# Performance work log

Hardware: AMD Instinct MI355X
Metric: run time of the kernel (lower is better)

Reference implementation:

```python
import jax, jax.numpy as jnp
import numpy as np

G, N, F_IN, D, R, E, L = 512, 128, 64, 128, 4, 1572864, 2  # graphs, nodes/graph, in-feat, embed, relations, edges, gnn layers


def setup_inputs() -> dict:
    key = jax.random.key(0)
    ks = jax.random.split(key, 8)
    x = jax.random.normal(ks[0], (G * N, F_IN), jnp.float32)
    # edges are within-graph (disjoint batched graph, as built by batch_to_gd)
    gid = jax.random.randint(ks[1], (E,), 0, G)
    loc = jax.random.randint(ks[2], (2, E), 0, N)
    edge_index = gid[None, :] * N + loc  # [2, E] (src, dst)
    edge_attr = jax.random.randint(ks[3], (E,), 0, R)
    W_emb = jax.random.normal(ks[4], (F_IN, D), jnp.float32) / np.sqrt(F_IN)
    b_emb = jnp.zeros((D,), jnp.float32)
    W_root = jax.random.normal(ks[5], (L, D, D), jnp.float32) / np.sqrt(D)
    W_rel = jax.random.normal(ks[6], (L, R, D, D), jnp.float32) / np.sqrt(D)
    bias = jnp.zeros((L, D), jnp.float32)
    return {"x": x, "edge_index": edge_index, "edge_attr": edge_attr,
            "W_emb": W_emb, "b_emb": b_emb, "W_root": W_root, "W_rel": W_rel, "bias": bias}


def rgcn_layer(h, edge_index, edge_attr, W_root_l, W_rel_l, bias_l):
    # PyG RGCNConv: out_i = h_i @ W_root + sum_r mean_{j in N_r(i)} (h_j @ W_r) + bias
    n = h.shape[0]
    xr = jnp.einsum('nd,rde->rne', h, W_rel_l)          # [R, n, D] per-relation transform
    src, dst = edge_index[0], edge_index[1]
    msg = xr[edge_attr, src]                             # [E, D] gather per edge
    seg = dst * R + edge_attr                            # combined (node, relation) segment id
    summed = jax.ops.segment_sum(msg, seg, num_segments=n * R)
    cnt = jax.ops.segment_sum(jnp.ones((msg.shape[0],), h.dtype), seg, num_segments=n * R)
    mean = summed / jnp.maximum(cnt, 1.0)[:, None]       # per-relation mean aggregation
    agg = mean.reshape(n, R, -1).sum(axis=1)             # sum over relations
    return h @ W_root_l + agg + bias_l


def reference(x, edge_index, edge_attr, W_emb, b_emb, W_root, W_rel, bias):
    h = x @ W_emb + b_emb                                # embedding_linear
    for l in range(L):                                   # mp_rounds = 1 per layer
        h = jax.nn.relu(rgcn_layer(h, edge_index, edge_attr, W_root[l], W_rel[l], bias[l]))
    # split into per-graph chunks of N nodes and max-pool over nodes
    return jnp.max(h.reshape(G, N, -1), axis=1)          # [G, D]
```

## Files before the change

### kernel.cpp

```cpp
#include <hip/hip_runtime.h>

constexpr int GG    = 512;
constexpr int NPG   = 128;
constexpr int FIN   = 64;
constexpr int DD    = 128;
constexpr int RR    = 4;
constexpr int NN    = GG * NPG;
constexpr int EE    = 1572864;
constexpr int SLC   = 4096;
constexpr int HSTR  = 136;
constexpr int BPAD  = 32;

typedef __attribute__((ext_vector_type(8))) _Float16 f16x8;
typedef __attribute__((ext_vector_type(2))) _Float16 f16x2;
typedef __attribute__((ext_vector_type(4))) float f32x4;
typedef unsigned short u16;
typedef unsigned int   u32;

__device__ __forceinline__ u16 f16b(float x) {
    _Float16 h = (_Float16)x;
    return __builtin_bit_cast(u16, h);
}
__device__ __forceinline__ f16x2 as2(u32 w) { return __builtin_bit_cast(f16x2, w); }

__device__ __forceinline__ void gl_lds16(const void* g, void* l) {
    __builtin_amdgcn_global_load_lds((const __attribute__((address_space(1))) u32*)g,
                                     (__attribute__((address_space(3))) u32*)l, 16, 0, 0);
}


__global__ __launch_bounds__(256, 2) void k_front(const int* __restrict__ ei,
                                                  const int* __restrict__ ea,
                                                  u32* __restrict__ bcur,
                                                  u16* __restrict__ binned,
                                                  const float* __restrict__ W_root,
                                                  const float* __restrict__ W_rel,
                                                  const float* __restrict__ W_emb,
                                                  u16* __restrict__ wtH) {
    __shared__ u32 sRec[4096];
    __shared__ int bh[512];
    __shared__ int lcur[512];
    __shared__ int lstart[512];
    __shared__ int gbase[512];
    __shared__ int wt4[4];
    __shared__ float tile[32 * 129];
    int tid = threadIdx.x;
    int bid = blockIdx.x;

    if (bid < 384) {
        int e0 = bid * 4096;
        bh[tid] = 0; bh[tid + 256] = 0;
        __syncthreads();
        for (int i = 0; i < 16; ++i) {
            int e = e0 + i * 256 + tid;
            int src = ei[e];
            int dst = ei[EE + e];
            int a   = ea[e];
            int g   = dst >> 7;
            u32 rec = (u32)(src & 127) | ((u32)(dst & 127) << 7) | ((u32)a << 14);
            sRec[i * 256 + tid] = rec | ((u32)g << 16);
            atomicAdd(&bh[g], 1);
        }
        __syncthreads();
        int c0 = bh[2 * tid], c1 = bh[2 * tid + 1];
        int s  = c0 + c1;
        int v  = s;
        int lane = tid & 63, wv = tid >> 6;
#pragma unroll
        for (int o = 1; o < 64; o <<= 1) {
            int t = __shfl_up(v, o);
            if (lane >= o) v += t;
        }
        if (lane == 63) wt4[wv] = v;
        gbase[2 * tid]     = (2 * tid) * SLC +
                             (int)atomicAdd(&bcur[(2 * tid) * BPAD], (u32)c0);
        gbase[2 * tid + 1] = (2 * tid + 1) * SLC +
                             (int)atomicAdd(&bcur[(2 * tid + 1) * BPAD], (u32)c1);
        __syncthreads();
        int base = 0;
#pragma unroll
        for (int w = 0; w < 4; ++w)
            if (w < wv) base += wt4[w];
        int ex = base + v - s;
        lstart[2 * tid]     = ex;
        lstart[2 * tid + 1] = ex + c0;
        lcur[2 * tid]       = ex;
        lcur[2 * tid + 1]   = ex + c0;
        __syncthreads();
        u32* sorted = (u32*)tile;
        for (int i = 0; i < 16; ++i) {
            u32 r = sRec[i * 256 + tid];
            int pos = atomicAdd(&lcur[r >> 16], 1);
            sorted[pos] = r;
        }
        __syncthreads();
        for (int i = 0; i < 16; ++i) {
            int p = i * 256 + tid;
            u32 r = sorted[p];
            int g = r >> 16;
            binned[gbase[g] + (p - lstart[g])] = (u16)(r & 0xFFFFu);
        }
    } else if (bid < 424) {
        int pb = bid - 384;
        int mat = pb >> 2;
        int k0 = (pb & 3) * 32;
        int l = mat / 5, m5 = mat - l * 5;
        const float* Wsrc = (m5 == 0) ? (W_root + l * 16384)
                                      : (W_rel + (size_t)(l * RR + (m5 - 1)) * 16384);
        for (int i = 0; i < 16; ++i) {
            int k = k0 + (tid >> 7) + i * 2;
            int n = tid & 127;
            tile[(k - k0) * 129 + n] = Wsrc[k * 128 + n];
        }
        __syncthreads();
        for (int i = 0; i < 16; ++i) {
            int kk = tid & 31;
            int n  = (tid >> 5) + i * 8;
            wtH[mat * 16384 + n * 128 + k0 + kk] = f16b(tile[kk * 129 + n]);
        }
    } else {
        int k0 = (bid - 424) * 32;
        for (int i = 0; i < 16; ++i) {
            int k = k0 + (tid >> 7) + i * 2;
            int n = tid & 127;
            tile[(k - k0) * 129 + n] = W_emb[k * 128 + n];
        }
        __syncthreads();
        for (int i = 0; i < 16; ++i) {
            int kk = tid & 31;
            int n  = (tid >> 5) + i * 8;
            wtH[163840 + n * 64 + k0 + kk] = f16b(tile[kk * 129 + n]);
        }
    }
}


__global__ __launch_bounds__(512, 4) void k_fused(const float* __restrict__ x,
                                                  const float* __restrict__ b_emb,
                                                  float* __restrict__ outF,
                                                  const u16* __restrict__ wtH,
                                                  const float* __restrict__ bias,
                                                  const u16* __restrict__ binned,
                                                  const u32* __restrict__ bcur) {
    __shared__ __align__(16) u16 hG[128 * HSTR];
    __shared__ __align__(16) u16 sQ[2][8192];
    __shared__ __align__(16) u16 sIdx[SLC];
    __shared__ int   sOffs[512];
    __shared__ int   sCnt[512];
    __shared__ float sInv[512];

    int tid  = threadIdx.x;
    int wave = tid >> 6, lane = tid & 63;
    int mm   = lane & 15;
    int qd   = lane >> 4;
    int gr   = blockIdx.x;
    int row0g = gr * NPG;
    int strip = wave * 16;
    const u16* wtE = wtH + 163840;

    auto stage = [&](int step, int bufi) {
        const u16* src = wtH + (step >> 1) * 16384 + (step & 1) * 64;
#pragma unroll
        for (int i = 0; i < 2; ++i) {
            int u = i * 512 + tid;
            int n = u >> 3, j = u & 7;
            gl_lds16(src + n * 128 + ((j ^ (n & 7)) * 8), &sQ[bufi][u * 8]);
        }
    };
    auto stageE = [&](int bufi) {
#pragma unroll
        for (int i = 0; i < 2; ++i) {
            int u = i * 512 + tid;
            int n = u >> 3, j = u & 7;
            gl_lds16(wtE + n * 64 + ((j ^ (n & 7)) * 8), &sQ[bufi][u * 8]);
        }
    };

    f32x4 acc[8];
    auto mfma_half = [&](int bufi, f16x8 A0, f16x8 A1) {
        const u16* buf = sQ[bufi];
#pragma unroll
        for (int nt = 0; nt < 8; ++nt) {
            int n = nt * 16 + mm;
            int g0 = n * 8 + ((0 * 4 + qd) ^ (n & 7));
            int g1 = n * 8 + ((1 * 4 + qd) ^ (n & 7));
            f16x8 B0 = *(const f16x8*)&buf[g0 * 8];
            f16x8 B1 = *(const f16x8*)&buf[g1 * 8];
            f32x4 a = acc[nt];
            a = __builtin_amdgcn_mfma_f32_16x16x32_f16(A0, B0, a, 0, 0, 0);
            a = __builtin_amdgcn_mfma_f32_16x16x32_f16(A1, B1, a, 0, 0, 0);
            acc[nt] = a;
        }
    };

    auto gather = [&](int rel, f16x8* AH) {
        int key = (rel << 7) + strip + mm;
        int r0 = sOffs[key];
        int r1 = sCnt[key];
        _Float16 hs = (_Float16)sInv[key];
        f16x2 sv; sv[0] = hs; sv[1] = hs;
        int cb = qd * 8;
        f16x2 ax[16];
#pragma unroll
        for (int i = 0; i < 16; ++i) ax[i] = (f16x2){(_Float16)0.f, (_Float16)0.f};
        auto add8 = [&](int ks, uint4 u) {
            ax[ks * 4 + 0] += as2(u.x);
            ax[ks * 4 + 1] += as2(u.y);
            ax[ks * 4 + 2] += as2(u.z);
            ax[ks * 4 + 3] += as2(u.w);
        };
        int j = r0;
        for (; j + 2 <= r1; j += 2) {
            int rb0 = (int)sIdx[j]     * HSTR + cb;
            int rb1 = (int)sIdx[j + 1] * HSTR + cb;
            uint4 a0 = *(const uint4*)&hG[rb0];
            uint4 a1 = *(const uint4*)&hG[rb0 + 32];
            uint4 a2 = *(const uint4*)&hG[rb0 + 64];
            uint4 a3 = *(const uint4*)&hG[rb0 + 96];
            uint4 b0 = *(const uint4*)&hG[rb1];
            uint4 b1 = *(const uint4*)&hG[rb1 + 32];
            uint4 b2 = *(const uint4*)&hG[rb1 + 64];
            uint4 b3 = *(const uint4*)&hG[rb1 + 96];
            add8(0, a0); add8(1, a1); add8(2, a2); add8(3, a3);
            add8(0, b0); add8(1, b1); add8(2, b2); add8(3, b3);
        }
        if (j < r1) {
            int rb = (int)sIdx[j] * HSTR + cb;
            uint4 a0 = *(const uint4*)&hG[rb];
            uint4 a1 = *(const uint4*)&hG[rb + 32];
            uint4 a2 = *(const uint4*)&hG[rb + 64];
            uint4 a3 = *(const uint4*)&hG[rb + 96];
            add8(0, a0); add8(1, a1); add8(2, a2); add8(3, a3);
        }
#pragma unroll
        for (int q = 0; q < 4; ++q) {
            union { u32 w[4]; f16x8 v; } o;
#pragma unroll
            for (int t = 0; t < 4; ++t) {
                f16x2 r = ax[q * 4 + t] * sv;
                o.w[t] = __builtin_bit_cast(u32, r);
            }
            AH[q] = o.v;
        }
    };

    stageE(0);
    int cnt = (int)bcur[gr * BPAD];
    if (cnt > SLC) cnt = SLC;
    uint4 myRec = *(const uint4*)&binned[gr * SLC + tid * 8];
    sCnt[tid] = 0;
    __syncthreads();
    int base8 = tid * 8;
#pragma unroll
    for (int i = 0; i < 8; ++i) {
        if (base8 + i < cnt) {
            u32 w = ((const u32*)&myRec)[i >> 1];
            u32 rec = (i & 1) ? (w >> 16) : (w & 0xFFFFu);
            atomicAdd(&sCnt[rec >> 7], 1);
        }
    }
    __syncthreads();
    int c = sCnt[tid];
    int v = c;
#pragma unroll
    for (int o = 1; o < 64; o <<= 1) {
        int t = __shfl_up(v, o);
        if (lane >= o) v += t;
    }
    int* wtot = (int*)sIdx;
    if (lane == 63) wtot[wave] = v;
    __syncthreads();
    int base = 0;
#pragma unroll
    for (int w = 0; w < 8; ++w) {
        int tw = wtot[w];
        if (w < wave) base += tw;
    }
    int ex = base + v - c;
    sOffs[tid] = ex;
    sCnt[tid]  = ex;
    sInv[tid]  = 1.0f / (float)(c > 0 ? c : 1);
    __syncthreads();
#pragma unroll
    for (int i = 0; i < 8; ++i) {
        if (base8 + i < cnt) {
            u32 w = ((const u32*)&myRec)[i >> 1];
            u32 rec = (i & 1) ? (w >> 16) : (w & 0xFFFFu);
            int pos = atomicAdd(&sCnt[rec >> 7], 1);
            sIdx[pos] = (u16)(rec & 127u);
        }
    }
    __syncthreads();

    {
#pragma unroll
        for (int nt = 0; nt < 8; ++nt) {
            float bv = b_emb[nt * 16 + mm];
            acc[nt] = (f32x4){bv, bv, bv, bv};
        }
        f16x8 AE[2];
#pragma unroll
        for (int ks = 0; ks < 2; ++ks) {
            const float* xp = &x[(size_t)(row0g + strip + mm) * FIN + ks * 32 + qd * 8];
            float4 a = *(const float4*)xp;
            float4 b = *(const float4*)(xp + 4);
            union { u32 w[4]; f16x8 v; } o;
            o.w[0] = (u32)f16b(a.x) | ((u32)f16b(a.y) << 16);
            o.w[1] = (u32)f16b(a.z) | ((u32)f16b(a.w) << 16);
            o.w[2] = (u32)f16b(b.x) | ((u32)f16b(b.y) << 16);
            o.w[3] = (u32)f16b(b.z) | ((u32)f16b(b.w) << 16);
            AE[ks] = o.v;
        }
        stage(0, 1);
        mfma_half(0, AE[0], AE[1]);
#pragma unroll
        for (int nt = 0; nt < 8; ++nt)
#pragma unroll
            for (int r = 0; r < 4; ++r)
                hG[(strip + qd * 4 + r) * HSTR + nt * 16 + mm] =
                    f16b(acc[nt][r]);
        __syncthreads();
    }

    for (int L = 0; L < 2; ++L) {
        const float* bl = bias + L * DD;
#pragma unroll
        for (int i = 0; i < 8; ++i) acc[i] = (f32x4){0.f, 0.f, 0.f, 0.f};

        f16x8 AH[4];
#pragma unroll
        for (int ks = 0; ks < 4; ++ks)
            AH[ks] = *(const f16x8*)&hG[(strip + mm) * HSTR + ks * 32 + qd * 8];

        for (int m = 0; m < 5; ++m) {
#pragma unroll
            for (int h = 0; h < 2; ++h) {
                int s = L * 10 + m * 2 + h;
                if (s + 1 < 20) stage(s + 1, s & 1);
                mfma_half((s + 1) & 1, AH[h * 2], AH[h * 2 + 1]);
                __syncthreads();
            }
            if (m < 4) gather(m, AH);
        }

        if (L == 0) {
#pragma unroll
            for (int nt = 0; nt < 8; ++nt) {
                float bv = bl[nt * 16 + mm];
#pragma unroll
                for (int r = 0; r < 4; ++r)
                    hG[(strip + qd * 4 + r) * HSTR + nt * 16 + mm] =
                        f16b(fmaxf(acc[nt][r] + bv, 0.f));
            }
            __syncthreads();
        } else {
            float* red = (float*)sIdx;
#pragma unroll
            for (int nt = 0; nt < 8; ++nt) {
                float bv = bl[nt * 16 + mm];
                float vv = fmaxf(fmaxf(acc[nt][0], acc[nt][1]),
                                 fmaxf(acc[nt][2], acc[nt][3])) + bv;
                vv = fmaxf(vv, 0.f);
                vv = fmaxf(vv, __shfl_xor(vv, 16));
                vv = fmaxf(vv, __shfl_xor(vv, 32));
                if (lane < 16) red[wave * 128 + nt * 16 + mm] = vv;
            }
            __syncthreads();
            if (tid < 128) {
                float mx = red[tid];
#pragma unroll
                for (int w = 1; w < 8; ++w) mx = fmaxf(mx, red[w * 128 + tid]);
                outF[gr * DD + tid] = mx;
            }
        }
    }
}


extern "C" void kernel_launch(void* const* d_in, const int* in_sizes, int n_in,
                              void* d_out, int out_size, void* d_ws, size_t ws_size,
                              hipStream_t stream) {
    const float* x      = (const float*)d_in[0];
    const int*   ei     = (const int*)  d_in[1];
    const int*   ea     = (const int*)  d_in[2];
    const float* W_emb  = (const float*)d_in[3];
    const float* b_emb  = (const float*)d_in[4];
    const float* W_root = (const float*)d_in[5];
    const float* W_rel  = (const float*)d_in[6];
    const float* bias   = (const float*)d_in[7];
    float* out = (float*)d_out;

    char* p = (char*)d_ws;
    u32* bcur   = (u32*)p; p += (size_t)512 * BPAD * 4;
    u16* binned = (u16*)p; p += (size_t)GG * SLC * 2;
    u16* wtH    = (u16*)p; p += (size_t)(10 * 16384 + 8192) * 2;

    (void)hipMemsetAsync(bcur, 0, (size_t)512 * BPAD * 4, stream);

    k_front<<<426, 256, 0, stream>>>(ei, ea, bcur, binned,
                                     W_root, W_rel, W_emb, wtH);
    k_fused<<<GG, 512, 0, stream>>>(x, b_emb, out, wtH, bias, binned, bcur);
}
```

Baseline: 162.2 us.

## Read weight B-operands directly from global memory instead of LDS double-buffer staging

Removes the LDS double-buffered weight staging (global_load_lds plus per-half barriers) and has each wave load MFMA B fragments straight from global/L2. This frees 32 KB of LDS and drops the per-step __syncthreads, and occupancy is raised from 4 to 6 blocks per CU via launch bounds. In exchange every wave re-fetches the full weight matrices from cache with uncoalesced-ish 16-byte loads, which adds L2/L1 traffic and latency. A leftover no-op lambda is also included.

```diff
diff --git a/kernel.cpp b/kernel.cpp
--- a/kernel.cpp
+++ b/kernel.cpp
@@ -22,11 +22,6 @@
     return __builtin_bit_cast(u16, h);
 }
 __device__ __forceinline__ f16x2 as2(u32 w) { return __builtin_bit_cast(f16x2, w); }
-
-__device__ __forceinline__ void gl_lds16(const void* g, void* l) {
-    __builtin_amdgcn_global_load_lds((const __attribute__((address_space(1))) u32*)g,
-                                     (__attribute__((address_space(3))) u32*)l, 16, 0, 0);
-}
 
 
 __global__ __launch_bounds__(256, 2) void k_front(const int* __restrict__ ei,
@@ -135,7 +130,7 @@
 }
 
 
-__global__ __launch_bounds__(512, 4) void k_fused(const float* __restrict__ x,
+__global__ __launch_bounds__(512, 6) void k_fused(const float* __restrict__ x,
                                                   const float* __restrict__ b_emb,
                                                   float* __restrict__ outF,
                                                   const u16* __restrict__ wtH,
@@ -143,7 +138,6 @@
                                                   const u16* __restrict__ binned,
                                                   const u32* __restrict__ bcur) {
     __shared__ __align__(16) u16 hG[128 * HSTR];
-    __shared__ __align__(16) u16 sQ[2][8192];
     __shared__ __align__(16) u16 sIdx[SLC];
     __shared__ int   sOffs[512];
     __shared__ int   sCnt[512];
@@ -158,40 +152,17 @@
     int strip = wave * 16;
     const u16* wtE = wtH + 163840;
 
-    auto stage = [&](int step, int bufi) {
-        const u16* src = wtH + (step >> 1) * 16384 + (step & 1) * 64;
-#pragma unroll
-        for (int i = 0; i < 2; ++i) {
-            int u = i * 512 + tid;
-            int n = u >> 3, j = u & 7;
-            gl_lds16(src + n * 128 + ((j ^ (n & 7)) * 8), &sQ[bufi][u * 8]);
+    f32x4 acc[8];
+
+    auto mat_mm = [&](const u16* base) {
+        const u16* bl = base + mm * 128 + qd * 8;
+#pragma unroll
+        for (int ks = 0; ks < 4; ++ks) {
+            f16x8 A;
+            (void)A;
         }
     };
-    auto stageE = [&](int bufi) {
-#pragma unroll
-        for (int i = 0; i < 2; ++i) {
-            int u = i * 512 + tid;
-            int n = u >> 3, j = u & 7;
-            gl_lds16(wtE + n * 64 + ((j ^ (n & 7)) * 8), &sQ[bufi][u * 8]);
-        }
-    };
-
-    f32x4 acc[8];
-    auto mfma_half = [&](int bufi, f16x8 A0, f16x8 A1) {
-        const u16* buf = sQ[bufi];
-#pragma unroll
-        for (int nt = 0; nt < 8; ++nt) {
-            int n = nt * 16 + mm;
-            int g0 = n * 8 + ((0 * 4 + qd) ^ (n & 7));
-            int g1 = n * 8 + ((1 * 4 + qd) ^ (n & 7));
-            f16x8 B0 = *(const f16x8*)&buf[g0 * 8];
-            f16x8 B1 = *(const f16x8*)&buf[g1 * 8];
-            f32x4 a = acc[nt];
-            a = __builtin_amdgcn_mfma_f32_16x16x32_f16(A0, B0, a, 0, 0, 0);
-            a = __builtin_amdgcn_mfma_f32_16x16x32_f16(A1, B1, a, 0, 0, 0);
-            acc[nt] = a;
-        }
-    };
+    (void)mat_mm;
 
     auto gather = [&](int rel, f16x8* AH) {
         int key = (rel << 7) + strip + mm;
@@ -244,7 +215,6 @@
         }
     };
 
-    stageE(0);
     int cnt = (int)bcur[gr * BPAD];
     if (cnt > SLC) cnt = SLC;
     uint4 myRec = *(const uint4*)&binned[gr * SLC + tid * 8];
@@ -311,8 +281,14 @@
             o.w[3] = (u32)f16b(b.z) | ((u32)f16b(b.w) << 16);
             AE[ks] = o.v;
         }
-        stage(0, 1);
-        mfma_half(0, AE[0], AE[1]);
+        const u16* bl = wtE + mm * 64 + qd * 8;
+#pragma unroll
+        for (int ks = 0; ks < 2; ++ks)
+#pragma unroll
+            for (int nt = 0; nt < 8; ++nt) {
+                f16x8 B = *(const f16x8*)&bl[nt * 16 * 64 + ks * 32];
+                acc[nt] = __builtin_amdgcn_mfma_f32_16x16x32_f16(AE[ks], B, acc[nt], 0, 0, 0);
+            }
 #pragma unroll
         for (int nt = 0; nt < 8; ++nt)
 #pragma unroll
@@ -333,15 +309,17 @@
             AH[ks] = *(const f16x8*)&hG[(strip + mm) * HSTR + ks * 32 + qd * 8];
 
         for (int m = 0; m < 5; ++m) {
-#pragma unroll
-            for (int h = 0; h < 2; ++h) {
-                int s = L * 10 + m * 2 + h;
-                if (s + 1 < 20) stage(s + 1, s & 1);
-                mfma_half((s + 1) & 1, AH[h * 2], AH[h * 2 + 1]);
-                __syncthreads();
-            }
+            const u16* mb = wtH + (size_t)(L * 5 + m) * 16384 + mm * 128 + qd * 8;
+#pragma unroll
+            for (int ks = 0; ks < 4; ++ks)
+#pragma unroll
+                for (int nt = 0; nt < 8; ++nt) {
+                    f16x8 B = *(const f16x8*)&mb[nt * 16 * 128 + ks * 32];
+                    acc[nt] = __builtin_amdgcn_mfma_f32_16x16x32_f16(AH[ks], B, acc[nt], 0, 0, 0);
+                }
             if (m < 4) gather(m, AH);
         }
+        __syncthreads();
 
         if (L == 0) {
 #pragma unroll
```

Result: slower. 282.1 us (+74.0%).

## Process two graphs per 1024-thread block sharing staged weight tiles

Applied to the files above, without the earlier changes.

Each block now handles two graphs with 1024 threads, with each half keeping its own node features, edge index bins and counters in LDS. The double-buffered weight tiles are shared by both halves and staged with one load per thread, which halves weight traffic and staging work per graph. The cost is block-wide barriers across both graphs, a grid of only 256 blocks on a GPU with many CUs, and more LDS per block, which may lower occupancy and leave load imbalance between the two graphs.

```diff
diff --git a/kernel.cpp b/kernel.cpp
--- a/kernel.cpp
+++ b/kernel.cpp
@@ -135,45 +135,45 @@
 }
 
 
-__global__ __launch_bounds__(512, 4) void k_fused(const float* __restrict__ x,
-                                                  const float* __restrict__ b_emb,
-                                                  float* __restrict__ outF,
-                                                  const u16* __restrict__ wtH,
-                                                  const float* __restrict__ bias,
-                                                  const u16* __restrict__ binned,
-                                                  const u32* __restrict__ bcur) {
-    __shared__ __align__(16) u16 hG[128 * HSTR];
+__global__ __launch_bounds__(1024, 4) void k_fused(const float* __restrict__ x,
+                                                   const float* __restrict__ b_emb,
+                                                   float* __restrict__ outF,
+                                                   const u16* __restrict__ wtH,
+                                                   const float* __restrict__ bias,
+                                                   const u16* __restrict__ binned,
+                                                   const u32* __restrict__ bcur) {
+    __shared__ __align__(16) u16 hG[2][128 * HSTR];
     __shared__ __align__(16) u16 sQ[2][8192];
-    __shared__ __align__(16) u16 sIdx[SLC];
-    __shared__ int   sOffs[512];
-    __shared__ int   sCnt[512];
-    __shared__ float sInv[512];
+    __shared__ __align__(16) u16 sIdx[2][SLC];
+    __shared__ int   sOffs[2][512];
+    __shared__ int   sCnt[2][512];
+    __shared__ float sInv[2][512];
 
     int tid  = threadIdx.x;
-    int wave = tid >> 6, lane = tid & 63;
+    int half = tid >> 9;
+    int htid = tid & 511;
+    int wave = htid >> 6, lane = tid & 63;
     int mm   = lane & 15;
     int qd   = lane >> 4;
-    int gr   = blockIdx.x;
+    int gr   = (blockIdx.x << 1) | half;
     int row0g = gr * NPG;
     int strip = wave * 16;
     const u16* wtE = wtH + 163840;
 
+    u16*   hGh   = hG[half];
+    u16*   sIdxh = sIdx[half];
+    int*   sOffsh = sOffs[half];
+    int*   sCnth  = sCnt[half];
+    float* sInvh  = sInv[half];
+
     auto stage = [&](int step, int bufi) {
         const u16* src = wtH + (step >> 1) * 16384 + (step & 1) * 64;
-#pragma unroll
-        for (int i = 0; i < 2; ++i) {
-            int u = i * 512 + tid;
-            int n = u >> 3, j = u & 7;
-            gl_lds16(src + n * 128 + ((j ^ (n & 7)) * 8), &sQ[bufi][u * 8]);
-        }
+        int n = tid >> 3, j = tid & 7;
+        gl_lds16(src + n * 128 + ((j ^ (n & 7)) * 8), &sQ[bufi][tid * 8]);
     };
     auto stageE = [&](int bufi) {
-#pragma unroll
-        for (int i = 0; i < 2; ++i) {
-            int u = i * 512 + tid;
-            int n = u >> 3, j = u & 7;
-            gl_lds16(wtE + n * 64 + ((j ^ (n & 7)) * 8), &sQ[bufi][u * 8]);
-        }
+        int n = tid >> 3, j = tid & 7;
+        gl_lds16(wtE + n * 64 + ((j ^ (n & 7)) * 8), &sQ[bufi][tid * 8]);
     };
 
     f32x4 acc[8];
@@ -195,9 +195,9 @@
 
     auto gather = [&](int rel, f16x8* AH) {
         int key = (rel << 7) + strip + mm;
-        int r0 = sOffs[key];
-        int r1 = sCnt[key];
-        _Float16 hs = (_Float16)sInv[key];
+        int r0 = sOffsh[key];
+        int r1 = sCnth[key];
+        _Float16 hs = (_Float16)sInvh[key];
         f16x2 sv; sv[0] = hs; sv[1] = hs;
         int cb = qd * 8;
         f16x2 ax[16];
@@ -211,25 +211,25 @@
         };
         int j = r0;
         for (; j + 2 <= r1; j += 2) {
-            int rb0 = (int)sIdx[j]     * HSTR + cb;
-            int rb1 = (int)sIdx[j + 1] * HSTR + cb;
-            uint4 a0 = *(const uint4*)&hG[rb0];
-            uint4 a1 = *(const uint4*)&hG[rb0 + 32];
-            uint4 a2 = *(const uint4*)&hG[rb0 + 64];
-            uint4 a3 = *(const uint4*)&hG[rb0 + 96];
-            uint4 b0 = *(const uint4*)&hG[rb1];
-            uint4 b1 = *(const uint4*)&hG[rb1 + 32];
-            uint4 b2 = *(const uint4*)&hG[rb1 + 64];
-            uint4 b3 = *(const uint4*)&hG[rb1 + 96];
+            int rb0 = (int)sIdxh[j]     * HSTR + cb;
+            int rb1 = (int)sIdxh[j + 1] * HSTR + cb;
+            uint4 a0 = *(const uint4*)&hGh[rb0];
+            uint4 a1 = *(const uint4*)&hGh[rb0 + 32];
+            uint4 a2 = *(const uint4*)&hGh[rb0 + 64];
+            uint4 a3 = *(const uint4*)&hGh[rb0 + 96];
+            uint4 b0 = *(const uint4*)&hGh[rb1];
+            uint4 b1 = *(const uint4*)&hGh[rb1 + 32];
+            uint4 b2 = *(const uint4*)&hGh[rb1 + 64];
+            uint4 b3 = *(const uint4*)&hGh[rb1 + 96];
             add8(0, a0); add8(1, a1); add8(2, a2); add8(3, a3);
             add8(0, b0); add8(1, b1); add8(2, b2); add8(3, b3);
         }
         if (j < r1) {
-            int rb = (int)sIdx[j] * HSTR + cb;
-            uint4 a0 = *(const uint4*)&hG[rb];
-            uint4 a1 = *(const uint4*)&hG[rb + 32];
-            uint4 a2 = *(const uint4*)&hG[rb + 64];
-            uint4 a3 = *(const uint4*)&hG[rb + 96];
+            int rb = (int)sIdxh[j] * HSTR + cb;
+            uint4 a0 = *(const uint4*)&hGh[rb];
+            uint4 a1 = *(const uint4*)&hGh[rb + 32];
+            uint4 a2 = *(const uint4*)&hGh[rb + 64];
+            uint4 a3 = *(const uint4*)&hGh[rb + 96];
             add8(0, a0); add8(1, a1); add8(2, a2); add8(3, a3);
         }
 #pragma unroll
@@ -247,27 +247,27 @@
     stageE(0);
     int cnt = (int)bcur[gr * BPAD];
     if (cnt > SLC) cnt = SLC;
-    uint4 myRec = *(const uint4*)&binned[gr * SLC + tid * 8];
-    sCnt[tid] = 0;
+    uint4 myRec = *(const uint4*)&binned[gr * SLC + htid * 8];
+    sCnth[htid] = 0;
     __syncthreads();
-    int base8 = tid * 8;
+    int base8 = htid * 8;
 #pragma unroll
     for (int i = 0; i < 8; ++i) {
         if (base8 + i < cnt) {
             u32 w = ((const u32*)&myRec)[i >> 1];
             u32 rec = (i & 1) ? (w >> 16) : (w & 0xFFFFu);
-            atomicAdd(&sCnt[rec >> 7], 1);
+            atomicAdd(&sCnth[rec >> 7], 1);
         }
     }
     __syncthreads();
-    int c = sCnt[tid];
+    int c = sCnth[htid];
     int v = c;
 #pragma unroll
     for (int o = 1; o < 64; o <<= 1) {
         int t = __shfl_up(v, o);
         if (lane >= o) v += t;
     }
-    int* wtot = (int*)sIdx;
+    int* wtot = (int*)sIdxh;
     if (lane == 63) wtot[wave] = v;
     __syncthreads();
     int base = 0;
@@ -277,17 +277,17 @@
         if (w < wave) base += tw;
     }
     int ex = base + v - c;
-    sOffs[tid] = ex;
-    sCnt[tid]  = ex;
-    sInv[tid]  = 1.0f / (float)(c > 0 ? c : 1);
+    sOffsh[htid] = ex;
+    sCnth[htid]  = ex;
+    sInvh[htid]  = 1.0f / (float)(c > 0 ? c : 1);
     __syncthreads();
 #pragma unroll
     for (int i = 0; i < 8; ++i) {
         if (base8 + i < cnt) {
             u32 w = ((const u32*)&myRec)[i >> 1];
             u32 rec = (i & 1) ? (w >> 16) : (w & 0xFFFFu);
-            int pos = atomicAdd(&sCnt[rec >> 7], 1);
-            sIdx[pos] = (u16)(rec & 127u);
+            int pos = atomicAdd(&sCnth[rec >> 7], 1);
+            sIdxh[pos] = (u16)(rec & 127u);
         }
     }
     __syncthreads();
@@ -317,7 +317,7 @@
         for (int nt = 0; nt < 8; ++nt)
 #pragma unroll
             for (int r = 0; r < 4; ++r)
-                hG[(strip + qd * 4 + r) * HSTR + nt * 16 + mm] =
+                hGh[(strip + qd * 4 + r) * HSTR + nt * 16 + mm] =
                     f16b(acc[nt][r]);
         __syncthreads();
     }
@@ -330,7 +330,7 @@
         f16x8 AH[4];
 #pragma unroll
         for (int ks = 0; ks < 4; ++ks)
-            AH[ks] = *(const f16x8*)&hG[(strip + mm) * HSTR + ks * 32 + qd * 8];
+            AH[ks] = *(const f16x8*)&hGh[(strip + mm) * HSTR + ks * 32 + qd * 8];
 
         for (int m = 0; m < 5; ++m) {
 #pragma unroll
@@ -349,12 +349,12 @@
                 float bv = bl[nt * 16 + mm];
 #pragma unroll
                 for (int r = 0; r < 4; ++r)
-                    hG[(strip + qd * 4 + r) * HSTR + nt * 16 + mm] =
+                    hGh[(strip + qd * 4 + r) * HSTR + nt * 16 + mm] =
                         f16b(fmaxf(acc[nt][r] + bv, 0.f));
             }
             __syncthreads();
         } else {
-            float* red = (float*)sIdx;
+            float* red = (float*)sIdxh;
 #pragma unroll
             for (int nt = 0; nt < 8; ++nt) {
                 float bv = bl[nt * 16 + mm];
@@ -366,11 +366,11 @@
                 if (lane < 16) red[wave * 128 + nt * 16 + mm] = vv;
             }
             __syncthreads();
-            if (tid < 128) {
-                float mx = red[tid];
-#pragma unroll
-                for (int w = 1; w < 8; ++w) mx = fmaxf(mx, red[w * 128 + tid]);
-                outF[gr * DD + tid] = mx;
+            if (htid < 128) {
+                float mx = red[htid];
+#pragma unroll
+                for (int w = 1; w < 8; ++w) mx = fmaxf(mx, red[w * 128 + htid]);
+                outF[gr * DD + htid] = mx;
             }
         }
     }
@@ -399,5 +399,5 @@
 
     k_front<<<426, 256, 0, stream>>>(ei, ea, bcur, binned,
                                      W_root, W_rel, W_emb, wtH);
-    k_fused<<<GG, 512, 0, stream>>>(x, b_emb, out, wtH, bias, binned, bcur);
+    k_fused<<<GG / 2, 1024, 0, stream>>>(x, b_emb, out, wtH, bias, binned, bcur);
 }
```

New measurement: 177.0 us. 9.1% more time.
